# Performance work log

Measured on AMD Instinct MI355X. Metric: run time of the kernel, lower is better.

## Reference

```python
import jax, jax.numpy as jnp
import numpy as np

DIM = 1024
HEADS = 16
N_SENTS = 64
N_ENTS = 16
BATCH = 32


def setup_inputs() -> dict:
    key = jax.random.key(0)
    ks = jax.random.split(key, 16)
    S, E, B, D = N_SENTS, N_ENTS, BATCH, DIM
    sc = 1.0 / np.sqrt(D)
    f32 = jnp.float32
    return {
        "entities": jax.random.normal(ks[0], (S * E, B, D), f32),
        "padding_mask": jnp.zeros((S * E, B), bool),
        "n_sents": S,
        # learned aggregation query, init uniform(-1, 1) as in the module
        "query": jax.random.uniform(ks[1], (1, 1, D), f32, -1.0, 1.0),
        # do_proj key/val Linear layers (torch Linear convention: y = x @ W.T + b)
        "Wk_lin": jax.random.normal(ks[2], (D, D), f32) * sc,
        "bk_lin": jnp.zeros((D,), f32),
        "Wv_lin": jax.random.normal(ks[3], (D, D), f32) * sc,
        "bv_lin": jnp.zeros((D,), f32),
        # MultiheadAttention in-projection (split q/k/v) and out-projection
        "Wq_in": jax.random.normal(ks[4], (D, D), f32) * sc,
        "bq_in": jnp.zeros((D,), f32),
        "Wk_in": jax.random.normal(ks[5], (D, D), f32) * sc,
        "bk_in": jnp.zeros((D,), f32),
        "Wv_in": jax.random.normal(ks[6], (D, D), f32) * sc,
        "bv_in": jnp.zeros((D,), f32),
        "Wo": jax.random.normal(ks[7], (D, D), f32) * sc,
        "bo": jnp.zeros((D,), f32),
    }


def reference(entities, padding_mask, n_sents, query,
              Wk_lin, bk_lin, Wv_lin, bv_lin,
              Wq_in, bq_in, Wk_in, bk_in, Wv_in, bv_in, Wo, bo):
    SE, B, D = entities.shape
    E = SE // n_sents
    H = HEADS
    hd = D // H

    # do_proj key/value linears
    keys = entities @ Wk_lin.T + bk_lin   # [SE, B, D]
    vals = entities @ Wv_lin.T + bv_lin   # [SE, B, D]

    # MHA in-projections. Query is a single learned vector shared across
    # sentences and batch, so project once: [H, hd], pre-scaled by 1/sqrt(hd).
    q = ((query[0, 0] @ Wq_in.T + bq_in).reshape(H, hd)) * (1.0 / np.sqrt(hd))
    # Honor the block-diagonal mask: query s only sees its n_ents key slice,
    # so reshape keys/vals to [S, E, B, H, hd] and never build [S, S*E] scores.
    k = (keys @ Wk_in.T + bk_in).reshape(n_sents, E, B, H, hd)
    v = (vals @ Wv_in.T + bv_in).reshape(n_sents, E, B, H, hd)

    scores = jnp.einsum('hd,sebhd->sbhe', q, k)            # [S, B, H, E]
    pm = padding_mask.reshape(n_sents, E, B).transpose(0, 2, 1)  # [S, B, E]
    scores = jnp.where(pm[:, :, None, :], -jnp.inf, scores)
    attn = jax.nn.softmax(scores, axis=-1)                 # [S, B, H, E]
    ctx = jnp.einsum('sbhe,sebhd->sbhd', attn, v).reshape(n_sents, B, D)
    return ctx @ Wo.T + bo                                  # [S, B, D]
```

## Files before the change

### kernel.cpp

```cpp
#include <hip/hip_runtime.h>
#include <hip/hip_bf16.h>

constexpr int kD  = 1024;
constexpr int kH  = 16;
constexpr int kHD = 64;
constexpr int kS  = 64;
constexpr int kE  = 16;
constexpr int kB  = 32;
constexpr int kSB = kS * kB;

typedef __attribute__((ext_vector_type(8))) short bfvec8;
typedef __attribute__((ext_vector_type(4))) float fvec4;

struct __align__(8)  bf4  { __hip_bfloat16 v[4]; };
struct __align__(16) bf8v { __hip_bfloat16 v[8]; };

__global__ __launch_bounds__(256) void k_pre2(const float* __restrict__ Wq_in,
                                              const float* __restrict__ query,
                                              const float* __restrict__ bq_in,
                                              const float* __restrict__ Wv_in,
                                              const float* __restrict__ bv_lin,
                                              const float* __restrict__ bv_in,
                                              const float* __restrict__ Wk_in,
                                              const float* __restrict__ bk_lin,
                                              const float* __restrict__ bk_in,
                                              const float* __restrict__ Wo,
                                              float* __restrict__ wmat,
                                              float* __restrict__ cvec,
                                              float* __restrict__ cb,
                                              __hip_bfloat16* __restrict__ Wobf) {
  int j = blockIdx.x, t = threadIdx.x;
  if (j < 64) {
    int h = j >> 2, chunk = j & 3;
    __shared__ float qs_s[64];
    __shared__ float kb2_s[64];
    int l = t & 63, w = t >> 6;
    int jj = w * 16 + (l >> 2);
    int part = l & 3;
    {
      const float4* w4 = (const float4*)(Wq_in + (size_t)(h * 64 + jj) * kD);
      const float4* q4 = (const float4*)query;
      float acc = 0.f;
      #pragma unroll 4
      for (int i = 0; i < 64; i++) {
        float4 a = w4[part + 4 * i], b = q4[part + 4 * i];
        acc += a.x * b.x + a.y * b.y + a.z * b.z + a.w * b.w;
      }
      acc += __shfl_xor(acc, 1);
      acc += __shfl_xor(acc, 2);
      if (part == 0) qs_s[jj] = (acc + bq_in[h * 64 + jj]) * 0.125f;
    }
    if (chunk == 0) {
      const float4* w4 = (const float4*)(Wk_in + (size_t)(h * 64 + jj) * kD);
      const float4* q4 = (const float4*)bk_lin;
      float acc = 0.f;
      #pragma unroll 4
      for (int i = 0; i < 64; i++) {
        float4 a = w4[part + 4 * i], b = q4[part + 4 * i];
        acc += a.x * b.x + a.y * b.y + a.z * b.z + a.w * b.w;
      }
      acc += __shfl_xor(acc, 1);
      acc += __shfl_xor(acc, 2);
      if (part == 0) kb2_s[jj] = acc + bk_in[h * 64 + jj];
    }
    __syncthreads();
    int d = chunk * 256 + t;
    float acc = 0.f;
    #pragma unroll 8
    for (int jr = 0; jr < 64; jr++)
      acc = fmaf(qs_s[jr], Wk_in[(size_t)(h * 64 + jr) * kD + d], acc);
    wmat[(size_t)h * kD + d] = acc;
    if (chunk == 0 && t < 64) {
      float v = qs_s[t] * kb2_s[t];
      #pragma unroll
      for (int o = 32; o >= 1; o >>= 1) v += __shfl_xor(v, o);
      if (t == 0) cvec[h] = v;
    }
    return;
  }
  if (j < 1088) {
    int row = j - 64;
    const float4* w4 = (const float4*)(Wv_in + (size_t)row * kD);
    const float4* v4 = (const float4*)bv_lin;
    float4 a = w4[t], b = v4[t];
    float acc = a.x * b.x + a.y * b.y + a.z * b.z + a.w * b.w;
    #pragma unroll
    for (int o = 32; o >= 1; o >>= 1) acc += __shfl_xor(acc, o);
    __shared__ float red[4];
    if ((t & 63) == 0) red[t >> 6] = acc;
    __syncthreads();
    if (t == 0) cb[row] = red[0] + red[1] + red[2] + red[3] + bv_in[row];
    return;
  }
  int i = (j - 1088) * kD + t * 4;
  float4 v = *(const float4*)(Wo + i);
  bf4 o;
  o.v[0] = __float2bfloat16(v.x); o.v[1] = __float2bfloat16(v.y);
  o.v[2] = __float2bfloat16(v.z); o.v[3] = __float2bfloat16(v.w);
  *(bf4*)(Wobf + i) = o;
}


__global__ __launch_bounds__(256) void k_attn_eagg(const float* __restrict__ ent,
                                                   const unsigned char* __restrict__ pmask,
                                                   const __hip_bfloat16* __restrict__ Ubf,
                                                   const float* __restrict__ cvec,
                                                   __hip_bfloat16* __restrict__ eagg) {
  __shared__ __hip_bfloat16 ent_s[kE][kD + 8];
  __shared__ float sred[4][kE][kH + 1];
  __shared__ __hip_bfloat16 attn_b[kH][32];
  int sb = blockIdx.x;
  int s = sb >> 5, b = sb & 31;
  int t = threadIdx.x, l = t & 63, w = t >> 6;
  int quad = l >> 4, lane16 = l & 15;

  const float* src = ent + (size_t)(s * kE) * kB * kD + (size_t)b * kD;
  #pragma unroll
  for (int it = 0; it < 8; it++) {
    int i = t + it * 256;
    int e = i >> 7, f = (i & 127) * 8;
    const float4* pp = (const float4*)(src + (size_t)e * kB * kD + f);
    float4 v0 = pp[0], v1 = pp[1];
    bf8v pk;
    pk.v[0] = __float2bfloat16(v0.x); pk.v[1] = __float2bfloat16(v0.y);
    pk.v[2] = __float2bfloat16(v0.z); pk.v[3] = __float2bfloat16(v0.w);
    pk.v[4] = __float2bfloat16(v1.x); pk.v[5] = __float2bfloat16(v1.y);
    pk.v[6] = __float2bfloat16(v1.z); pk.v[7] = __float2bfloat16(v1.w);
    *(bf8v*)&ent_s[e][f] = pk;
  }
  __syncthreads();

  fvec4 sacc = {};
  #pragma unroll
  for (int ks = 0; ks < 8; ks++) {
    int k0 = w * 256 + ks * 32 + quad * 8;
    bfvec8 a = *(const bfvec8*)&ent_s[lane16][k0];
    bfvec8 bb = *(const bfvec8*)&Ubf[(size_t)lane16 * kD + k0];
    sacc = __builtin_amdgcn_mfma_f32_16x16x32_bf16(a, bb, sacc, 0, 0, 0);
  }
  #pragma unroll
  for (int i = 0; i < 4; i++) sred[w][quad * 4 + i][lane16] = sacc[i];
  __syncthreads();

  {
    int h = t >> 4, e = t & 15;
    float sc = sred[0][e][h] + sred[1][e][h] + sred[2][e][h] + sred[3][e][h] + cvec[h];
    if (pmask[(size_t)(s * kE + e) * kB + b]) sc = -INFINITY;
    float m = sc;
    #pragma unroll
    for (int o = 8; o >= 1; o >>= 1) m = fmaxf(m, __shfl_xor(m, o, 16));
    float ex = __expf(sc - m);
    float sum = ex;
    #pragma unroll
    for (int o = 8; o >= 1; o >>= 1) sum += __shfl_xor(sum, o, 16);
    attn_b[h][e] = __float2bfloat16(ex / sum);
    attn_b[h][e + 16] = __float2bfloat16(0.f);
  }
  __syncthreads();

  bfvec8 bfrag = *(const bfvec8*)&attn_b[lane16][quad * 8];
  __hip_bfloat16* dst = eagg + (size_t)sb * (kH * kD);
  for (int tt = 0; tt < 16; tt++) {
    int dme = (w * 16 + tt) * 16 + lane16;
    bfvec8 afrag = {};
    if (quad < 2) {
      #pragma unroll
      for (int j = 0; j < 8; j++)
        afrag[j] = *(const short*)&ent_s[quad * 8 + j][dme];
    }
    fvec4 acc = {};
    acc = __builtin_amdgcn_mfma_f32_16x16x32_bf16(afrag, bfrag, acc, 0, 0, 0);
    int d0 = (w * 16 + tt) * 16 + quad * 4;
    bf4 o;
    o.v[0] = __float2bfloat16(acc[0]); o.v[1] = __float2bfloat16(acc[1]);
    o.v[2] = __float2bfloat16(acc[2]); o.v[3] = __float2bfloat16(acc[3]);
    *(bf4*)&dst[(size_t)lane16 * kD + d0] = o;
  }
}


__device__ __forceinline__ void stage_row(const __hip_bfloat16* g, __hip_bfloat16* s) {
  *(bf8v*)s = *(const bf8v*)g;
}
__device__ __forceinline__ void stage_row(const float* g, __hip_bfloat16* s) {
  const float4* p = (const float4*)g;
  float4 v0 = p[0], v1 = p[1];
  bf8v pk;
  pk.v[0] = __float2bfloat16(v0.x); pk.v[1] = __float2bfloat16(v0.y);
  pk.v[2] = __float2bfloat16(v0.z); pk.v[3] = __float2bfloat16(v0.w);
  pk.v[4] = __float2bfloat16(v1.x); pk.v[5] = __float2bfloat16(v1.y);
  pk.v[6] = __float2bfloat16(v1.z); pk.v[7] = __float2bfloat16(v1.w);
  *(bf8v*)s = pk;
}


template <int MODE, typename TA, typename TB, typename TC>
__global__ __launch_bounds__(256) void k_gemm_mfma(
    const TA* __restrict__ Abase, int lda, long aBatch,
    const TB* __restrict__ Bbase, int ldb, long bBatch,
    TC* __restrict__ Cbase, int ldc, long cBatch,
    const float* __restrict__ bias, long biasBatch, int Ksz) {
  const TA* Ag = Abase + (size_t)blockIdx.z * aBatch;
  const TB* Bg = Bbase + (size_t)blockIdx.z * bBatch;
  TC* Cg = Cbase + (size_t)blockIdx.z * cBatch;
  const float* biasp = bias ? bias + (size_t)blockIdx.z * biasBatch : nullptr;
  const int m0 = blockIdx.x * 64, n0 = blockIdx.y * 64;
  __shared__ __hip_bfloat16 As[64][72];
  __shared__ __hip_bfloat16 Bs[64][72];
  const int t = threadIdx.x;
  const int l = t & 63, w = t >> 6;
  const int quad = l >> 4, col = l & 15;
  fvec4 acc[4] = {};
  for (int k0 = 0; k0 < Ksz; k0 += 64) {
    #pragma unroll
    for (int c = t; c < 512; c += 256) {
      int row = c >> 3, kq = (c & 7) * 8;
      stage_row(Ag + (size_t)(m0 + row) * lda + k0 + kq, &As[row][kq]);
      stage_row(Bg + (size_t)(n0 + row) * ldb + k0 + kq, &Bs[row][kq]);
    }
    __syncthreads();
    #pragma unroll
    for (int ks = 0; ks < 64; ks += 32) {
      bfvec8 a = *(const bfvec8*)&As[w * 16 + col][ks + quad * 8];
      #pragma unroll
      for (int nt = 0; nt < 4; nt++) {
        bfvec8 b = *(const bfvec8*)&Bs[nt * 16 + col][ks + quad * 8];
        acc[nt] = __builtin_amdgcn_mfma_f32_16x16x32_bf16(a, b, acc[nt], 0, 0, 0);
      }
    }
    __syncthreads();
  }
  #pragma unroll
  for (int nt = 0; nt < 4; nt++) {
    int n = n0 + nt * 16 + col;
    float bv = biasp ? biasp[n] : 0.f;
    #pragma unroll
    for (int i = 0; i < 4; i++) {
      int r = m0 + w * 16 + quad * 4 + i;
      float v = acc[nt][i] + bv;
      if constexpr (MODE == 0) ((float*)Cg)[(size_t)r * ldc + n] = v;
      else ((__hip_bfloat16*)Cg)[(size_t)r * ldc + n] = __float2bfloat16(v);
    }
  }
}


__global__ __launch_bounds__(256) void k_gemm_nn(
    const float* __restrict__ A0, const float* __restrict__ B0,
    __hip_bfloat16* __restrict__ C0,
    const float* __restrict__ A1, const float* __restrict__ B1,
    __hip_bfloat16* __restrict__ C1, int Ksz) {
  const bool isU = (blockIdx.x == 16);
  const float* Ag = isU ? A1 : A0;
  const float* Bg = isU ? B1 : B0;
  __hip_bfloat16* Cg = isU ? C1 : C0;
  const int m0 = isU ? 0 : blockIdx.x * 64, n0 = blockIdx.y * 64;
  __shared__ __hip_bfloat16 As[64][72];
  __shared__ __hip_bfloat16 Bs[64][72];
  const int t = threadIdx.x;
  const int l = t & 63, w = t >> 6;
  const int quad = l >> 4, col = l & 15;
  fvec4 acc[4] = {};
  for (int k0 = 0; k0 < Ksz; k0 += 64) {
    #pragma unroll
    for (int c = t; c < 512; c += 256) {
      int row = c >> 3, kq = (c & 7) * 8;
      stage_row(Ag + (size_t)(m0 + row) * kD + k0 + kq, &As[row][kq]);
      const float4* pb = (const float4*)(Bg + (size_t)(k0 + row) * kD + n0 + kq);
      float4 b0 = pb[0], b1 = pb[1];
      Bs[kq + 0][row] = __float2bfloat16(b0.x);
      Bs[kq + 1][row] = __float2bfloat16(b0.y);
      Bs[kq + 2][row] = __float2bfloat16(b0.z);
      Bs[kq + 3][row] = __float2bfloat16(b0.w);
      Bs[kq + 4][row] = __float2bfloat16(b1.x);
      Bs[kq + 5][row] = __float2bfloat16(b1.y);
      Bs[kq + 6][row] = __float2bfloat16(b1.z);
      Bs[kq + 7][row] = __float2bfloat16(b1.w);
    }
    __syncthreads();
    #pragma unroll
    for (int ks = 0; ks < 64; ks += 32) {
      bfvec8 a = *(const bfvec8*)&As[w * 16 + col][ks + quad * 8];
      #pragma unroll
      for (int nt = 0; nt < 4; nt++) {
        bfvec8 b = *(const bfvec8*)&Bs[nt * 16 + col][ks + quad * 8];
        acc[nt] = __builtin_amdgcn_mfma_f32_16x16x32_bf16(a, b, acc[nt], 0, 0, 0);
      }
    }
    __syncthreads();
  }
  #pragma unroll
  for (int nt = 0; nt < 4; nt++) {
    int n = n0 + nt * 16 + col;
    #pragma unroll
    for (int i = 0; i < 4; i++) {
      int r = m0 + w * 16 + quad * 4 + i;
      Cg[(size_t)r * kD + n] = __float2bfloat16(acc[nt][i]);
    }
  }
}

extern "C" void kernel_launch(void* const* d_in, const int* in_sizes, int n_in,
                              void* d_out, int out_size, void* d_ws, size_t ws_size,
                              hipStream_t stream) {
  const float* ent            = (const float*)d_in[0];
  const unsigned char* pmask  = (const unsigned char*)d_in[1];
  const float* query          = (const float*)d_in[3];
  const float* Wk_lin         = (const float*)d_in[4];
  const float* bk_lin         = (const float*)d_in[5];
  const float* Wv_lin         = (const float*)d_in[6];
  const float* bv_lin         = (const float*)d_in[7];
  const float* Wq_in          = (const float*)d_in[8];
  const float* bq_in          = (const float*)d_in[9];
  const float* Wk_in          = (const float*)d_in[10];
  const float* bk_in          = (const float*)d_in[11];
  const float* Wv_in          = (const float*)d_in[12];
  const float* bv_in          = (const float*)d_in[13];
  const float* Wo             = (const float*)d_in[14];
  const float* bo             = (const float*)d_in[15];
  float* out = (float*)d_out;

  float* p = (float*)d_ws;
  float* wmat = p; p += 64 * kD;
  float* cvec = p; p += 256;
  float* cb   = p; p += kD;
  __hip_bfloat16* bp = (__hip_bfloat16*)p;
  __hip_bfloat16* Ubf  = bp; bp += (size_t)64 * kD;
  __hip_bfloat16* Mmat = bp; bp += (size_t)kD * kD;
  __hip_bfloat16* Wobf = bp; bp += (size_t)kD * kD;
  __hip_bfloat16* ctx2 = bp; bp += (size_t)kSB * kD;
  __hip_bfloat16* eagg = bp;

  k_pre2<<<2112, 256, 0, stream>>>(Wq_in, query, bq_in, Wv_in, bv_lin, bv_in,
                                   Wk_in, bk_lin, bk_in, Wo,
                                   wmat, cvec, cb, Wobf);
  k_gemm_nn<<<dim3(17, 16, 1), 256, 0, stream>>>(Wv_in, Wv_lin, Mmat,
                                                 wmat, Wk_lin, Ubf, kD);
  k_attn_eagg<<<kSB, 256, 0, stream>>>(ent, pmask, Ubf, cvec, eagg);
  k_gemm_mfma<2, __hip_bfloat16, __hip_bfloat16, __hip_bfloat16>
      <<<dim3(kSB / 64, 1, kH), 256, 0, stream>>>(
      eagg, kH * kD, (long)kD, Mmat, kD, (long)(kHD * kD),
      ctx2, kD, (long)kHD, cb, (long)kHD, kD);
  k_gemm_mfma<0, __hip_bfloat16, __hip_bfloat16, float>
      <<<dim3(kSB / 64, kD / 64, 1), 256, 0, stream>>>(
      ctx2, kD, 0L, Wobf, kD, 0L, out, kD, 0L, bo, 0L, kD);
}
```

Before: 337.5 us.

## Double GEMM K-tile to 128 with XOR-swizzled shared memory layout

Both MFMA GEMM kernels now stage 128-wide K tiles per iteration instead of 64, which halves the number of barrier-separated loop trips. The padded LDS arrays are replaced by unpadded 128-column tiles that use an XOR swizzle on 8-element chunks to avoid bank conflicts on the vector reads. The transposed-B staging in k_gemm_nn uses a matching swizzle on its scalar writes. LDS use per block doubles, which may lower occupancy, and the swizzle indexing adds integer work.

New measurement: 344.5 us. 1.02x slower.

```diff
diff --git a/kernel.cpp b/kernel.cpp
--- a/kernel.cpp
+++ b/kernel.cpp
@@ -205,26 +205,30 @@
   TC* Cg = Cbase + (size_t)blockIdx.z * cBatch;
   const float* biasp = bias ? bias + (size_t)blockIdx.z * biasBatch : nullptr;
   const int m0 = blockIdx.x * 64, n0 = blockIdx.y * 64;
-  __shared__ __hip_bfloat16 As[64][72];
-  __shared__ __hip_bfloat16 Bs[64][72];
+  __shared__ __hip_bfloat16 As[64 * 128];
+  __shared__ __hip_bfloat16 Bs[64 * 128];
   const int t = threadIdx.x;
   const int l = t & 63, w = t >> 6;
   const int quad = l >> 4, col = l & 15;
   fvec4 acc[4] = {};
-  for (int k0 = 0; k0 < Ksz; k0 += 64) {
-    #pragma unroll
-    for (int c = t; c < 512; c += 256) {
-      int row = c >> 3, kq = (c & 7) * 8;
-      stage_row(Ag + (size_t)(m0 + row) * lda + k0 + kq, &As[row][kq]);
-      stage_row(Bg + (size_t)(n0 + row) * ldb + k0 + kq, &Bs[row][kq]);
-    }
-    __syncthreads();
-    #pragma unroll
-    for (int ks = 0; ks < 64; ks += 32) {
-      bfvec8 a = *(const bfvec8*)&As[w * 16 + col][ks + quad * 8];
+  for (int k0 = 0; k0 < Ksz; k0 += 128) {
+    #pragma unroll
+    for (int c = t; c < 1024; c += 256) {
+      int row = c >> 4, sl = c & 15;
+      int so = row * 128 + ((sl ^ (row & 7)) << 3);
+      stage_row(Ag + (size_t)(m0 + row) * lda + k0 + sl * 8, &As[so]);
+      stage_row(Bg + (size_t)(n0 + row) * ldb + k0 + sl * 8, &Bs[so]);
+    }
+    __syncthreads();
+    #pragma unroll
+    for (int ks = 0; ks < 128; ks += 32) {
+      int kb = (ks >> 3) + quad;
+      int arow = w * 16 + col;
+      bfvec8 a = *(const bfvec8*)&As[arow * 128 + ((kb ^ (arow & 7)) << 3)];
       #pragma unroll
       for (int nt = 0; nt < 4; nt++) {
-        bfvec8 b = *(const bfvec8*)&Bs[nt * 16 + col][ks + quad * 8];
+        int brow = nt * 16 + col;
+        bfvec8 b = *(const bfvec8*)&Bs[brow * 128 + ((kb ^ (brow & 7)) << 3)];
         acc[nt] = __builtin_amdgcn_mfma_f32_16x16x32_bf16(a, b, acc[nt], 0, 0, 0);
       }
     }
@@ -255,35 +259,41 @@
   const float* Bg = isU ? B1 : B0;
   __hip_bfloat16* Cg = isU ? C1 : C0;
   const int m0 = isU ? 0 : blockIdx.x * 64, n0 = blockIdx.y * 64;
-  __shared__ __hip_bfloat16 As[64][72];
-  __shared__ __hip_bfloat16 Bs[64][72];
+  __shared__ __hip_bfloat16 As[64 * 128];
+  __shared__ __hip_bfloat16 Bs[64 * 128];
   const int t = threadIdx.x;
   const int l = t & 63, w = t >> 6;
   const int quad = l >> 4, col = l & 15;
   fvec4 acc[4] = {};
-  for (int k0 = 0; k0 < Ksz; k0 += 64) {
-    #pragma unroll
-    for (int c = t; c < 512; c += 256) {
-      int row = c >> 3, kq = (c & 7) * 8;
-      stage_row(Ag + (size_t)(m0 + row) * kD + k0 + kq, &As[row][kq]);
-      const float4* pb = (const float4*)(Bg + (size_t)(k0 + row) * kD + n0 + kq);
+  for (int k0 = 0; k0 < Ksz; k0 += 128) {
+    #pragma unroll
+    for (int c = t; c < 1024; c += 256) {
+      int row = c >> 4, sl = c & 15;
+      stage_row(Ag + (size_t)(m0 + row) * kD + k0 + sl * 8,
+                &As[row * 128 + ((sl ^ (row & 7)) << 3)]);
+    }
+    #pragma unroll
+    for (int c = t; c < 1024; c += 256) {
+      int krow = c >> 3, nq = (c & 7) * 8;
+      const float4* pb = (const float4*)(Bg + (size_t)(k0 + krow) * kD + n0 + nq);
       float4 b0 = pb[0], b1 = pb[1];
-      Bs[kq + 0][row] = __float2bfloat16(b0.x);
-      Bs[kq + 1][row] = __float2bfloat16(b0.y);
-      Bs[kq + 2][row] = __float2bfloat16(b0.z);
-      Bs[kq + 3][row] = __float2bfloat16(b0.w);
-      Bs[kq + 4][row] = __float2bfloat16(b1.x);
-      Bs[kq + 5][row] = __float2bfloat16(b1.y);
-      Bs[kq + 6][row] = __float2bfloat16(b1.z);
-      Bs[kq + 7][row] = __float2bfloat16(b1.w);
-    }
-    __syncthreads();
-    #pragma unroll
-    for (int ks = 0; ks < 64; ks += 32) {
-      bfvec8 a = *(const bfvec8*)&As[w * 16 + col][ks + quad * 8];
+      float bv[8] = {b0.x, b0.y, b0.z, b0.w, b1.x, b1.y, b1.z, b1.w};
+      #pragma unroll
+      for (int i = 0; i < 8; i++) {
+        int n = nq + i;
+        Bs[n * 128 + (krow ^ (((n >> 3) & 7) << 3))] = __float2bfloat16(bv[i]);
+      }
+    }
+    __syncthreads();
+    #pragma unroll
+    for (int ks = 0; ks < 128; ks += 32) {
+      int kb = (ks >> 3) + quad;
+      int arow = w * 16 + col;
+      bfvec8 a = *(const bfvec8*)&As[arow * 128 + ((kb ^ (arow & 7)) << 3)];
       #pragma unroll
       for (int nt = 0; nt < 4; nt++) {
-        bfvec8 b = *(const bfvec8*)&Bs[nt * 16 + col][ks + quad * 8];
+        int brow = nt * 16 + col;
+        bfvec8 b = *(const bfvec8*)&Bs[brow * 128 + ((kb ^ ((brow >> 3) & 7)) << 3)];
         acc[nt] = __builtin_amdgcn_mfma_f32_16x16x32_bf16(a, b, acc[nt], 0, 0, 0);
       }
     }
```

## Split-K all GEMMs four ways with fp32 atomic accumulation

Applied to the files above, without the earlier changes.

Each GEMM (weight-fold, ctx, output projection) now splits its K dimension into four chunks across extra blocks and accumulates into fp32 buffers with atomicAdd. A zeroing kernel and a final bias kernel are added, and intermediates (M, U, ctx) become fp32 that is converted to bf16 when staged. The aim is more blocks for small grids (e.g. the ctx GEMM had only 512 blocks), at the cost of atomic traffic, larger fp32 intermediates, extra zeroing, two more launches, and nondeterministic summation order.

After: 370.1 us. 1.1x slower.

```diff
diff --git a/kernel.cpp b/kernel.cpp
--- a/kernel.cpp
+++ b/kernel.cpp
@@ -14,6 +14,12 @@
 
 struct __align__(8)  bf4  { __hip_bfloat16 v[4]; };
 struct __align__(16) bf8v { __hip_bfloat16 v[8]; };
+
+__global__ __launch_bounds__(256) void k_zero(float* __restrict__ p, int n4) {
+  int stride = gridDim.x * 256;
+  for (int i = blockIdx.x * 256 + threadIdx.x; i < n4; i += stride)
+    *(float4*)(p + (size_t)i * 4) = float4{0.f, 0.f, 0.f, 0.f};
+}
 
 __global__ __launch_bounds__(256) void k_pre2(const float* __restrict__ Wq_in,
                                               const float* __restrict__ query,
@@ -100,10 +106,19 @@
   *(bf4*)(Wobf + i) = o;
 }
 
+__device__ __forceinline__ bfvec8 f8_to_bf(float4 a, float4 b) {
+  bf8v pk;
+  pk.v[0] = __float2bfloat16(a.x); pk.v[1] = __float2bfloat16(a.y);
+  pk.v[2] = __float2bfloat16(a.z); pk.v[3] = __float2bfloat16(a.w);
+  pk.v[4] = __float2bfloat16(b.x); pk.v[5] = __float2bfloat16(b.y);
+  pk.v[6] = __float2bfloat16(b.z); pk.v[7] = __float2bfloat16(b.w);
+  return *(bfvec8*)&pk;
+}
+
 
 __global__ __launch_bounds__(256) void k_attn_eagg(const float* __restrict__ ent,
                                                    const unsigned char* __restrict__ pmask,
-                                                   const __hip_bfloat16* __restrict__ Ubf,
+                                                   const float* __restrict__ Uacc,
                                                    const float* __restrict__ cvec,
                                                    __hip_bfloat16* __restrict__ eagg) {
   __shared__ __hip_bfloat16 ent_s[kE][kD + 8];
@@ -135,7 +150,9 @@
   for (int ks = 0; ks < 8; ks++) {
     int k0 = w * 256 + ks * 32 + quad * 8;
     bfvec8 a = *(const bfvec8*)&ent_s[lane16][k0];
-    bfvec8 bb = *(const bfvec8*)&Ubf[(size_t)lane16 * kD + k0];
+    const float* up = Uacc + (size_t)lane16 * kD + k0;
+    float4 u0 = *(const float4*)up, u1 = *(const float4*)(up + 4);
+    bfvec8 bb = f8_to_bf(u0, u1);
     sacc = __builtin_amdgcn_mfma_f32_16x16x32_bf16(a, bb, sacc, 0, 0, 0);
   }
   #pragma unroll
@@ -194,16 +211,17 @@
 }
 
 
-template <int MODE, typename TA, typename TB, typename TC>
-__global__ __launch_bounds__(256) void k_gemm_mfma(
+template <typename TA, typename TB>
+__global__ __launch_bounds__(256) void k_gemm_sk(
     const TA* __restrict__ Abase, int lda, long aBatch,
     const TB* __restrict__ Bbase, int ldb, long bBatch,
-    TC* __restrict__ Cbase, int ldc, long cBatch,
+    float* __restrict__ Cbase, int ldc, long cBatch,
     const float* __restrict__ bias, long biasBatch, int Ksz) {
-  const TA* Ag = Abase + (size_t)blockIdx.z * aBatch;
-  const TB* Bg = Bbase + (size_t)blockIdx.z * bBatch;
-  TC* Cg = Cbase + (size_t)blockIdx.z * cBatch;
-  const float* biasp = bias ? bias + (size_t)blockIdx.z * biasBatch : nullptr;
+  const int bz = blockIdx.z >> 2, sk = blockIdx.z & 3;
+  const TA* Ag = Abase + (size_t)bz * aBatch;
+  const TB* Bg = Bbase + (size_t)bz * bBatch;
+  float* Cg = Cbase + (size_t)bz * cBatch;
+  const float* biasp = (bias && sk == 0) ? bias + (size_t)bz * biasBatch : nullptr;
   const int m0 = blockIdx.x * 64, n0 = blockIdx.y * 64;
   __shared__ __hip_bfloat16 As[64][72];
   __shared__ __hip_bfloat16 Bs[64][72];
@@ -211,7 +229,8 @@
   const int l = t & 63, w = t >> 6;
   const int quad = l >> 4, col = l & 15;
   fvec4 acc[4] = {};
-  for (int k0 = 0; k0 < Ksz; k0 += 64) {
+  const int kc = Ksz >> 2;
+  for (int k0 = sk * kc; k0 < sk * kc + kc; k0 += 64) {
     #pragma unroll
     for (int c = t; c < 512; c += 256) {
       int row = c >> 3, kq = (c & 7) * 8;
@@ -237,23 +256,22 @@
     #pragma unroll
     for (int i = 0; i < 4; i++) {
       int r = m0 + w * 16 + quad * 4 + i;
-      float v = acc[nt][i] + bv;
-      if constexpr (MODE == 0) ((float*)Cg)[(size_t)r * ldc + n] = v;
-      else ((__hip_bfloat16*)Cg)[(size_t)r * ldc + n] = __float2bfloat16(v);
-    }
-  }
-}
-
-
-__global__ __launch_bounds__(256) void k_gemm_nn(
+      atomicAdd(&Cg[(size_t)r * ldc + n], acc[nt][i] + bv);
+    }
+  }
+}
+
+
+__global__ __launch_bounds__(256) void k_gemm_nn_sk(
     const float* __restrict__ A0, const float* __restrict__ B0,
-    __hip_bfloat16* __restrict__ C0,
+    float* __restrict__ C0,
     const float* __restrict__ A1, const float* __restrict__ B1,
-    __hip_bfloat16* __restrict__ C1, int Ksz) {
+    float* __restrict__ C1, int Ksz) {
   const bool isU = (blockIdx.x == 16);
+  const int sk = blockIdx.z;
   const float* Ag = isU ? A1 : A0;
   const float* Bg = isU ? B1 : B0;
-  __hip_bfloat16* Cg = isU ? C1 : C0;
+  float* Cg = isU ? C1 : C0;
   const int m0 = isU ? 0 : blockIdx.x * 64, n0 = blockIdx.y * 64;
   __shared__ __hip_bfloat16 As[64][72];
   __shared__ __hip_bfloat16 Bs[64][72];
@@ -261,7 +279,8 @@
   const int l = t & 63, w = t >> 6;
   const int quad = l >> 4, col = l & 15;
   fvec4 acc[4] = {};
-  for (int k0 = 0; k0 < Ksz; k0 += 64) {
+  const int kc = Ksz >> 2;
+  for (int k0 = sk * kc; k0 < sk * kc + kc; k0 += 64) {
     #pragma unroll
     for (int c = t; c < 512; c += 256) {
       int row = c >> 3, kq = (c & 7) * 8;
@@ -295,9 +314,19 @@
     #pragma unroll
     for (int i = 0; i < 4; i++) {
       int r = m0 + w * 16 + quad * 4 + i;
-      Cg[(size_t)r * kD + n] = __float2bfloat16(acc[nt][i]);
-    }
-  }
+      atomicAdd(&Cg[(size_t)r * kD + n], acc[nt][i]);
+    }
+  }
+}
+
+__global__ __launch_bounds__(256) void k_bias(const float* __restrict__ accp,
+                                              const float* __restrict__ bo,
+                                              float* __restrict__ out) {
+  int i = (blockIdx.x * 256 + threadIdx.x) * 4;
+  float4 v = *(const float4*)(accp + i);
+  float4 bv = *(const float4*)(bo + (i & (kD - 1)));
+  v.x += bv.x; v.y += bv.y; v.z += bv.z; v.w += bv.w;
+  *(float4*)(out + i) = v;
 }
 
 extern "C" void kernel_launch(void* const* d_in, const int* in_sizes, int n_in,
@@ -324,24 +353,27 @@
   float* wmat = p; p += 64 * kD;
   float* cvec = p; p += 256;
   float* cb   = p; p += kD;
+  float* accbase = p;
+  float* Macc   = p; p += (size_t)kD * kD;
+  float* Uacc   = p; p += (size_t)64 * kD;
+  float* ctxacc = p; p += (size_t)kSB * kD;
+  float* outacc = p; p += (size_t)kSB * kD;
+  int zero_n4 = (int)(((size_t)kD * kD + 64 * kD + 2 * (size_t)kSB * kD) / 4);
   __hip_bfloat16* bp = (__hip_bfloat16*)p;
-  __hip_bfloat16* Ubf  = bp; bp += (size_t)64 * kD;
-  __hip_bfloat16* Mmat = bp; bp += (size_t)kD * kD;
   __hip_bfloat16* Wobf = bp; bp += (size_t)kD * kD;
-  __hip_bfloat16* ctx2 = bp; bp += (size_t)kSB * kD;
   __hip_bfloat16* eagg = bp;
 
+  k_zero<<<2048, 256, 0, stream>>>(accbase, zero_n4);
   k_pre2<<<2112, 256, 0, stream>>>(Wq_in, query, bq_in, Wv_in, bv_lin, bv_in,
                                    Wk_in, bk_lin, bk_in, Wo,
                                    wmat, cvec, cb, Wobf);
-  k_gemm_nn<<<dim3(17, 16, 1), 256, 0, stream>>>(Wv_in, Wv_lin, Mmat,
-                                                 wmat, Wk_lin, Ubf, kD);
-  k_attn_eagg<<<kSB, 256, 0, stream>>>(ent, pmask, Ubf, cvec, eagg);
-  k_gemm_mfma<2, __hip_bfloat16, __hip_bfloat16, __hip_bfloat16>
-      <<<dim3(kSB / 64, 1, kH), 256, 0, stream>>>(
-      eagg, kH * kD, (long)kD, Mmat, kD, (long)(kHD * kD),
-      ctx2, kD, (long)kHD, cb, (long)kHD, kD);
-  k_gemm_mfma<0, __hip_bfloat16, __hip_bfloat16, float>
-      <<<dim3(kSB / 64, kD / 64, 1), 256, 0, stream>>>(
-      ctx2, kD, 0L, Wobf, kD, 0L, out, kD, 0L, bo, 0L, kD);
-}
+  k_gemm_nn_sk<<<dim3(17, 16, 4), 256, 0, stream>>>(Wv_in, Wv_lin, Macc,
+                                                    wmat, Wk_lin, Uacc, kD);
+  k_attn_eagg<<<kSB, 256, 0, stream>>>(ent, pmask, Uacc, cvec, eagg);
+  k_gemm_sk<__hip_bfloat16, float><<<dim3(kSB / 64, 1, kH * 4), 256, 0, stream>>>(
+      eagg, kH * kD, (long)kD, Macc, kD, (long)(kHD * kD),
+      ctxacc, kD, (long)kHD, cb, (long)kHD, kD);
+  k_gemm_sk<float, __hip_bfloat16><<<dim3(kSB / 64, kD / 64, 4), 256, 0, stream>>>(
+      ctxacc, kD, 0L, Wobf, kD, 0L, outacc, kD, 0L, nullptr, 0L, kD);
+  k_bias<<<kSB * kD / 1024, 256, 0, stream>>>(outacc, bo, out);
+}
```
